# Performance work log

Hardware: AMD Instinct MI355X
Metric: run time of the kernel (lower is better)

Reference implementation:

```python
import jax, jax.numpy as jnp
import numpy as np

T, B, I, H = 512, 256, 256, 512  # seq_len, batch, input_size, hidden_size


def setup_inputs() -> dict:
    key = jax.random.key(0)
    ks = jax.random.split(key, 7)
    sc = 1.0 / np.sqrt(H)  # PyTorch nn.RNN init scale ~ U(-1/sqrt(H), 1/sqrt(H)); use scaled normal
    return {
        "x": jax.random.normal(ks[0], (T, B, I), dtype=jnp.float32),
        "w_ih": jax.random.normal(ks[1], (H, I), dtype=jnp.float32) * sc,
        "w_hh": jax.random.normal(ks[2], (H, H), dtype=jnp.float32) * sc,
        "b_ih": jax.random.normal(ks[3], (H,), dtype=jnp.float32) * sc,
        "b_hh": jax.random.normal(ks[4], (H,), dtype=jnp.float32) * sc,
        "w_fc": jax.random.normal(ks[5], (I, H), dtype=jnp.float32) * sc,
        "b_fc": jax.random.normal(ks[6], (I,), dtype=jnp.float32) * sc,
    }


def reference(x, w_ih, w_hh, b_ih, b_hh, w_fc, b_fc):
    # Single-layer tanh RNN (h0 = 0): h_t = tanh(x_t W_ih^T + b_ih + h_{t-1} W_hh^T + b_hh)
    # Hoist the input projection out of the recurrence (one big GEMM).
    xp = jnp.einsum('tbi,hi->tbh', x, w_ih) + b_ih + b_hh  # [T,B,H]
    h0 = jnp.zeros((x.shape[1], w_hh.shape[0]), dtype=x.dtype)

    def step(h, xt):
        h_new = jnp.tanh(xt + h @ w_hh.T)
        return h_new, h_new

    _, hs = jax.lax.scan(step, h0, xp)  # hs: [T,B,H]
    # Output head: Linear(hidden_size -> input_size)
    return jnp.einsum('tbh,oh->tbo', hs, w_fc) + b_fc  # [T,B,I]
```

## Files before the change

### kernel.cpp

```cpp
#include <hip/hip_runtime.h>
#include <hip/hip_bf16.h>

#define T_ 512
#define B_ 256
#define I_ 256
#define H_ 512

#define NG 16
#define NS 4

#define RING_WPG (H_ * 8)
#define RING_BYTES (2ull * NG * RING_WPG * 8)

typedef _Float16 f16x8 __attribute__((ext_vector_type(8)));
typedef float f32x4 __attribute__((ext_vector_type(4)));

__device__ __forceinline__ float tanh_fast(float v) {
  float e = __expf(2.0f * v);
  return 1.0f - 2.0f / (e + 1.0f);
}

__device__ __forceinline__ f16x8 cvt8(const float4 a, const float4 b) {
  f16x8 f;
  f[0] = (_Float16)a.x; f[1] = (_Float16)a.y; f[2] = (_Float16)a.z; f[3] = (_Float16)a.w;
  f[4] = (_Float16)b.x; f[5] = (_Float16)b.y; f[6] = (_Float16)b.z; f[7] = (_Float16)b.w;
  return f;
}

__device__ __forceinline__ unsigned long long pack2h(_Float16 a, _Float16 b, unsigned tag) {
  unsigned ua = __builtin_bit_cast(unsigned short, a);
  unsigned ub = __builtin_bit_cast(unsigned short, b);
  return (unsigned long long)(ua | (ub << 16)) | ((unsigned long long)tag << 32);
}

__global__ __launch_bounds__(256, 1) void rnn_recurrence(
    const float* __restrict__ x,
    const float* __restrict__ w_ih,
    const float* __restrict__ w_hh,
    const float* __restrict__ b_ih,
    const float* __restrict__ b_hh,
    unsigned long long* __restrict__ ring,
    unsigned long long* __restrict__ ringf,
    _Float16* __restrict__ hs)
{
  const int tid  = threadIdx.x;
  const int lane = tid & 63;
  const int w    = tid >> 6;
  const int bid  = blockIdx.x;
  const int g    = bid & 15;
  const int s    = bid >> 4;
  const int r0   = g * 16;
  const int c0   = s * 128;
  const int lrow = lane & 15;
  const int quad = lane >> 4;
  const int kq   = quad * 8;

  __shared__ _Float16 hbuf[16][512 + 8];
  __shared__ _Float16 xbuf[16][256 + 8];
  __shared__ int g_ok;

  f16x8 whh0[16], whh1[16];
  f16x8 wih0[8], wih1[8];
  const int n0c = c0 + (2 * w + 0) * 16 + lrow;
  const int n1c = c0 + (2 * w + 1) * 16 + lrow;
  const float bias0 = b_ih[n0c] + b_hh[n0c];
  const float bias1 = b_ih[n1c] + b_hh[n1c];
  #pragma unroll
  for (int kt = 0; kt < 16; ++kt) {
    const int pk = (s * 4 + kt) & 15;
    const int k  = pk * 32 + kq;
    whh0[kt] = cvt8(*(const float4*)(w_hh + (size_t)n0c * H_ + k),
                    *(const float4*)(w_hh + (size_t)n0c * H_ + k + 4));
    whh1[kt] = cvt8(*(const float4*)(w_hh + (size_t)n1c * H_ + k),
                    *(const float4*)(w_hh + (size_t)n1c * H_ + k + 4));
  }
  #pragma unroll
  for (int kt = 0; kt < 8; ++kt) {
    const int k = kt * 32 + kq;
    wih0[kt] = cvt8(*(const float4*)(w_ih + (size_t)n0c * I_ + k),
                    *(const float4*)(w_ih + (size_t)n0c * I_ + k + 4));
    wih1[kt] = cvt8(*(const float4*)(w_ih + (size_t)n1c * I_ + k),
                    *(const float4*)(w_ih + (size_t)n1c * I_ + k + 4));
  }

  int roff[12];
  int obyte[12];
  #pragma unroll
  for (int j = 0; j < 12; ++j) {
    const int wdx = tid + j * 256;
    const int rs  = wdx >> 10;
    const int sl  = rs + (rs >= s ? 1 : 0);
    const int c   = (wdx >> 3) & 127;
    const int p   = wdx & 7;
    roff[j]  = (sl * 128 + c) * 8 + p;
    obyte[j] = roff[j] * 8;
  }

  if (tid == 0) g_ok = 1;
  {
    const int row = tid >> 4, ch = tid & 15;
    f16x8 z = {0, 0, 0, 0, 0, 0, 0, 0};
    *(f16x8*)(&hbuf[row][c0 + ch * 8]) = z;
  }
  __syncthreads();

  bool fastmode = true;
  const int xrow = tid >> 5;
  const int xcol = (tid & 31) * 8;

  for (int t = 0; t < T_; ++t) {
    const unsigned ut = (unsigned)t;
    const size_t slot_c = (size_t)((t & 1) ? NG : 0) + g;
    const size_t slot_p = (size_t)(((t + 1) & 1) ? NG : 0) + g;

    const float* src = x + ((size_t)t * B_ + r0) * I_;
    const float4 xv0 = *(const float4*)(src + (size_t)xrow * I_ + xcol);
    const float4 xv1 = *(const float4*)(src + (size_t)xrow * I_ + xcol + 4);
    const float4 xv2 = *(const float4*)(src + (size_t)(xrow + 8) * I_ + xcol);
    const float4 xv3 = *(const float4*)(src + (size_t)(xrow + 8) * I_ + xcol + 4);

    if (t > 0) {
      const int row = tid >> 4, ch = tid & 15;
      *(uint4*)(hs + ((size_t)(t - 1) * B_ + r0 + row) * H_ + c0 + ch * 8) =
          *(const uint4*)(&hbuf[row][c0 + ch * 8]);
    }

    f32x4 a0a = {0.f,0.f,0.f,0.f}, a0b = {0.f,0.f,0.f,0.f};
    f32x4 a1a = {0.f,0.f,0.f,0.f}, a1b = {0.f,0.f,0.f,0.f};
    #pragma unroll
    for (int kt = 0; kt < 4; ++kt) {
      const int pk = (s * 4 + kt) & 15;
      const f16x8 a = *(const f16x8*)(&hbuf[lrow][pk * 32 + kq]);
      a0b = __builtin_amdgcn_mfma_f32_16x16x32_f16(a, whh0[kt], a0b, 0, 0, 0);
      a1b = __builtin_amdgcn_mfma_f32_16x16x32_f16(a, whh1[kt], a1b, 0, 0, 0);
    }

    *(f16x8*)(&xbuf[xrow][xcol])     = cvt8(xv0, xv1);
    *(f16x8*)(&xbuf[xrow + 8][xcol]) = cvt8(xv2, xv3);

    unsigned long long v[12];
    unsigned miss = 0xfffu;
    if (fastmode) {
      const unsigned long long* fb = ringf + slot_c * RING_WPG;
      const int limit = (t <= 1) ? 256 : 0x7fffffff;
      int rounds = 0;
      do {
        asm volatile(
            "global_load_dwordx2 %0, %13, %12 sc0\n\t"
            "global_load_dwordx2 %1, %14, %12 sc0\n\t"
            "global_load_dwordx2 %2, %15, %12 sc0\n\t"
            "global_load_dwordx2 %3, %16, %12 sc0\n\t"
            "global_load_dwordx2 %4, %17, %12 sc0\n\t"
            "global_load_dwordx2 %5, %18, %12 sc0\n\t"
            "global_load_dwordx2 %6, %19, %12 sc0\n\t"
            "global_load_dwordx2 %7, %20, %12 sc0\n\t"
            "global_load_dwordx2 %8, %21, %12 sc0\n\t"
            "global_load_dwordx2 %9, %22, %12 sc0\n\t"
            "global_load_dwordx2 %10, %23, %12 sc0\n\t"
            "global_load_dwordx2 %11, %24, %12 sc0\n\t"
            "s_waitcnt vmcnt(0)"
            : "=&v"(v[0]), "=&v"(v[1]), "=&v"(v[2]), "=&v"(v[3]),
              "=&v"(v[4]), "=&v"(v[5]), "=&v"(v[6]), "=&v"(v[7]),
              "=&v"(v[8]), "=&v"(v[9]), "=&v"(v[10]), "=&v"(v[11])
            : "s"(fb), "v"(obyte[0]), "v"(obyte[1]), "v"(obyte[2]),
              "v"(obyte[3]), "v"(obyte[4]), "v"(obyte[5]), "v"(obyte[6]),
              "v"(obyte[7]), "v"(obyte[8]), "v"(obyte[9]), "v"(obyte[10]),
              "v"(obyte[11])
            : "memory");
        miss = 0u;
        #pragma unroll
        for (int j = 0; j < 12; ++j)
          if ((unsigned)(v[j] >> 32) != ut) miss |= 1u << j;
      } while (miss && ++rounds < limit);
      if (miss) g_ok = 0;
    }
    if (miss) {
      const unsigned long long* rg = ring + slot_c * RING_WPG;
      while (miss) {
        #pragma unroll
        for (int j = 0; j < 12; ++j) {
          if (miss & (1u << j)) {
            const unsigned long long wv = __hip_atomic_load(
                &rg[roff[j]], __ATOMIC_RELAXED, __HIP_MEMORY_SCOPE_AGENT);
            if ((unsigned)(wv >> 32) == ut) { v[j] = wv; miss &= ~(1u << j); }
          }
        }
      }
    }
    #pragma unroll
    for (int j = 0; j < 12; ++j) {
      const int col = roff[j] >> 3;
      const int pr  = (roff[j] & 7) * 2;
      const unsigned lo = (unsigned)v[j];
      hbuf[pr + 0][col] =
          __builtin_bit_cast(_Float16, (unsigned short)(lo & 0xffff));
      hbuf[pr + 1][col] =
          __builtin_bit_cast(_Float16, (unsigned short)(lo >> 16));
    }
    __syncthreads();
    if (t == 1) fastmode = (g_ok != 0);

    #pragma unroll
    for (int kt = 4; kt < 16; ++kt) {
      const int pk = (s * 4 + kt) & 15;
      const f16x8 a = *(const f16x8*)(&hbuf[lrow][pk * 32 + kq]);
      if (kt < 10) {
        a0a = __builtin_amdgcn_mfma_f32_16x16x32_f16(a, whh0[kt], a0a, 0, 0, 0);
        a1a = __builtin_amdgcn_mfma_f32_16x16x32_f16(a, whh1[kt], a1a, 0, 0, 0);
      } else {
        a0b = __builtin_amdgcn_mfma_f32_16x16x32_f16(a, whh0[kt], a0b, 0, 0, 0);
        a1b = __builtin_amdgcn_mfma_f32_16x16x32_f16(a, whh1[kt], a1b, 0, 0, 0);
      }
    }
    #pragma unroll
    for (int kt = 0; kt < 8; ++kt) {
      const f16x8 a = *(const f16x8*)(&xbuf[lrow][kt * 32 + kq]);
      if (kt < 4) {
        a0a = __builtin_amdgcn_mfma_f32_16x16x32_f16(a, wih0[kt], a0a, 0, 0, 0);
        a1a = __builtin_amdgcn_mfma_f32_16x16x32_f16(a, wih1[kt], a1a, 0, 0, 0);
      } else {
        a0b = __builtin_amdgcn_mfma_f32_16x16x32_f16(a, wih0[kt], a0b, 0, 0, 0);
        a1b = __builtin_amdgcn_mfma_f32_16x16x32_f16(a, wih1[kt], a1b, 0, 0, 0);
      }
    }
    const f32x4 acc0 = a0a + a0b;
    const f32x4 acc1 = a1a + a1b;

    _Float16 e0[4], e1[4];
    #pragma unroll
    for (int r = 0; r < 4; ++r) {
      e0[r] = (_Float16)tanh_fast(acc0[r] + bias0);
      e1[r] = (_Float16)tanh_fast(acc1[r] + bias1);
    }
    const unsigned tag = (unsigned)(t + 1);
    if (fastmode) {
      unsigned long long* fn = ringf + slot_p * RING_WPG;
      fn[n0c * 8 + quad * 2 + 0] = pack2h(e0[0], e0[1], tag);
      fn[n0c * 8 + quad * 2 + 1] = pack2h(e0[2], e0[3], tag);
      fn[n1c * 8 + quad * 2 + 0] = pack2h(e1[0], e1[1], tag);
      fn[n1c * 8 + quad * 2 + 1] = pack2h(e1[2], e1[3], tag);
    }
    if (t == 0 || !fastmode) {
      unsigned long long* rn = ring + slot_p * RING_WPG;
      __hip_atomic_store(&rn[n0c * 8 + quad * 2 + 0], pack2h(e0[0], e0[1], tag),
                         __ATOMIC_RELAXED, __HIP_MEMORY_SCOPE_AGENT);
      __hip_atomic_store(&rn[n0c * 8 + quad * 2 + 1], pack2h(e0[2], e0[3], tag),
                         __ATOMIC_RELAXED, __HIP_MEMORY_SCOPE_AGENT);
      __hip_atomic_store(&rn[n1c * 8 + quad * 2 + 0], pack2h(e1[0], e1[1], tag),
                         __ATOMIC_RELAXED, __HIP_MEMORY_SCOPE_AGENT);
      __hip_atomic_store(&rn[n1c * 8 + quad * 2 + 1], pack2h(e1[2], e1[3], tag),
                         __ATOMIC_RELAXED, __HIP_MEMORY_SCOPE_AGENT);
    }
    #pragma unroll
    for (int r = 0; r < 4; ++r) {
      hbuf[quad * 4 + r][n0c] = e0[r];
      hbuf[quad * 4 + r][n1c] = e1[r];
    }
    __syncthreads();
  }

  {
    const int row = tid >> 4, ch = tid & 15;
    *(uint4*)(hs + ((size_t)(T_ - 1) * B_ + r0 + row) * H_ + c0 + ch * 8) =
        *(const uint4*)(&hbuf[row][c0 + ch * 8]);
  }
}

__global__ __launch_bounds__(256) void fc_head(
    const _Float16* __restrict__ hs,
    const float* __restrict__ w_fc,
    const float* __restrict__ b_fc,
    float* __restrict__ out)
{
  const int tid  = threadIdx.x;
  const int lane = tid & 63;
  const int w    = tid >> 6;
  const int wm   = w & 1;
  const int wn   = w >> 1;
  const int m0   = blockIdx.y * 64;
  const int n0   = blockIdx.x * 64;
  const int lrow = lane & 15;
  const int quad = lane >> 4;
  const int kq   = quad * 8;

  __shared__ _Float16 As[64][32 + 8];
  __shared__ _Float16 Bs[64][32 + 8];

  f32x4 acc00 = {0.f,0.f,0.f,0.f}, acc01 = {0.f,0.f,0.f,0.f};
  f32x4 acc10 = {0.f,0.f,0.f,0.f}, acc11 = {0.f,0.f,0.f,0.f};

  const int srow = tid >> 2;
  const int skc  = (tid & 3) * 8;

  for (int k0 = 0; k0 < H_; k0 += 32) {
    *(uint4*)(&As[srow][skc]) =
        *(const uint4*)(hs + (size_t)(m0 + srow) * H_ + k0 + skc);
    *(f16x8*)(&Bs[srow][skc]) =
        cvt8(*(const float4*)(w_fc + (size_t)(n0 + srow) * H_ + k0 + skc),
             *(const float4*)(w_fc + (size_t)(n0 + srow) * H_ + k0 + skc + 4));
    __syncthreads();

    const f16x8 a0 = *(const f16x8*)(&As[wm * 32 + lrow][kq]);
    const f16x8 a1 = *(const f16x8*)(&As[wm * 32 + 16 + lrow][kq]);
    const f16x8 b0 = *(const f16x8*)(&Bs[wn * 32 + lrow][kq]);
    const f16x8 b1 = *(const f16x8*)(&Bs[wn * 32 + 16 + lrow][kq]);
    acc00 = __builtin_amdgcn_mfma_f32_16x16x32_f16(a0, b0, acc00, 0, 0, 0);
    acc01 = __builtin_amdgcn_mfma_f32_16x16x32_f16(a0, b1, acc01, 0, 0, 0);
    acc10 = __builtin_amdgcn_mfma_f32_16x16x32_f16(a1, b0, acc10, 0, 0, 0);
    acc11 = __builtin_amdgcn_mfma_f32_16x16x32_f16(a1, b1, acc11, 0, 0, 0);
    __syncthreads();
  }

  #pragma unroll
  for (int ni = 0; ni < 2; ++ni) {
    const int col = n0 + wn * 32 + ni * 16 + lrow;
    const float bf = b_fc[col];
    #pragma unroll
    for (int mi = 0; mi < 2; ++mi) {
      const f32x4 a = (mi == 0) ? (ni == 0 ? acc00 : acc01)
                                : (ni == 0 ? acc10 : acc11);
      #pragma unroll
      for (int r = 0; r < 4; ++r) {
        const int rowm = m0 + wm * 32 + mi * 16 + quad * 4 + r;
        out[(size_t)rowm * I_ + col] = a[r] + bf;
      }
    }
  }
}

extern "C" void kernel_launch(void* const* d_in, const int* in_sizes, int n_in,
                              void* d_out, int out_size, void* d_ws, size_t ws_size,
                              hipStream_t stream) {
  const float* x    = (const float*)d_in[0];
  const float* w_ih = (const float*)d_in[1];
  const float* w_hh = (const float*)d_in[2];
  const float* b_ih = (const float*)d_in[3];
  const float* b_hh = (const float*)d_in[4];
  const float* w_fc = (const float*)d_in[5];
  const float* b_fc = (const float*)d_in[6];
  float* out = (float*)d_out;

  unsigned long long* ring  = (unsigned long long*)d_ws;
  unsigned long long* ringf = (unsigned long long*)((char*)d_ws + RING_BYTES);
  _Float16* hs = (_Float16*)((char*)d_ws + 2 * RING_BYTES);

  hipMemsetAsync(d_ws, 0, 2 * RING_BYTES, stream);

  rnn_recurrence<<<64, 256, 0, stream>>>(x, w_ih, w_hh, b_ih, b_hh, ring, ringf, hs);
  fc_head<<<dim3(4, 2048), 256, 0, stream>>>(hs, w_fc, b_fc, out);
}
```

Baseline: 1.706 ms.

## Hoist input projection into a separate GEMM and prefetch xp in recurrence

Moves the x·W_ih^T input projection (with both biases) out of the serial recurrence into a parallel fp16 GEMM kernel that writes xp into the output buffer as scratch. The recurrence then loads precomputed xp values into the accumulator init, prefetching the next step's values, and drops the per-step W_ih MFMAs, x loads and xbuf staging. The fast/slow ring mode handling is also changed: the shared flag becomes a per-thread retry budget, both rings are always written, and __syncthreads is replaced by a raw barrier with an lgkm wait. The cost is an extra launch and an fp16 xp round-trip through HBM, and xp is rounded to fp16 before being added to the hidden-state product.

```diff
diff --git a/kernel.cpp b/kernel.cpp
--- a/kernel.cpp
+++ b/kernel.cpp
@@ -33,12 +33,79 @@
   return (unsigned long long)(ua | (ub << 16)) | ((unsigned long long)tag << 32);
 }
 
-__global__ __launch_bounds__(256, 1) void rnn_recurrence(
+__device__ __forceinline__ void barrier_lgkm() {
+  asm volatile("s_waitcnt lgkmcnt(0)" ::: "memory");
+  __builtin_amdgcn_s_barrier();
+  __builtin_amdgcn_sched_barrier(0);
+}
+
+__global__ __launch_bounds__(256) void xp_gemm(
     const float* __restrict__ x,
     const float* __restrict__ w_ih,
-    const float* __restrict__ w_hh,
     const float* __restrict__ b_ih,
     const float* __restrict__ b_hh,
+    _Float16* __restrict__ xp)
+{
+  const int tid  = threadIdx.x;
+  const int lane = tid & 63;
+  const int w    = tid >> 6;
+  const int wm   = w & 1;
+  const int wn   = w >> 1;
+  const int m0   = blockIdx.y * 64;
+  const int n0   = blockIdx.x * 64;
+  const int lrow = lane & 15;
+  const int quad = lane >> 4;
+  const int kq   = quad * 8;
+
+  __shared__ _Float16 As[64][32 + 8];
+  __shared__ _Float16 Bs[64][32 + 8];
+
+  f32x4 acc00 = {0.f,0.f,0.f,0.f}, acc01 = {0.f,0.f,0.f,0.f};
+  f32x4 acc10 = {0.f,0.f,0.f,0.f}, acc11 = {0.f,0.f,0.f,0.f};
+
+  const int srow = tid >> 2;
+  const int skc  = (tid & 3) * 8;
+
+  for (int k0 = 0; k0 < I_; k0 += 32) {
+    *(f16x8*)(&As[srow][skc]) =
+        cvt8(*(const float4*)(x + (size_t)(m0 + srow) * I_ + k0 + skc),
+             *(const float4*)(x + (size_t)(m0 + srow) * I_ + k0 + skc + 4));
+    *(f16x8*)(&Bs[srow][skc]) =
+        cvt8(*(const float4*)(w_ih + (size_t)(n0 + srow) * I_ + k0 + skc),
+             *(const float4*)(w_ih + (size_t)(n0 + srow) * I_ + k0 + skc + 4));
+    __syncthreads();
+
+    const f16x8 a0 = *(const f16x8*)(&As[wm * 32 + lrow][kq]);
+    const f16x8 a1 = *(const f16x8*)(&As[wm * 32 + 16 + lrow][kq]);
+    const f16x8 b0 = *(const f16x8*)(&Bs[wn * 32 + lrow][kq]);
+    const f16x8 b1 = *(const f16x8*)(&Bs[wn * 32 + 16 + lrow][kq]);
+    acc00 = __builtin_amdgcn_mfma_f32_16x16x32_f16(a0, b0, acc00, 0, 0, 0);
+    acc01 = __builtin_amdgcn_mfma_f32_16x16x32_f16(a0, b1, acc01, 0, 0, 0);
+    acc10 = __builtin_amdgcn_mfma_f32_16x16x32_f16(a1, b0, acc10, 0, 0, 0);
+    acc11 = __builtin_amdgcn_mfma_f32_16x16x32_f16(a1, b1, acc11, 0, 0, 0);
+    __syncthreads();
+  }
+
+  #pragma unroll
+  for (int ni = 0; ni < 2; ++ni) {
+    const int col = n0 + wn * 32 + ni * 16 + lrow;
+    const float bf = b_ih[col] + b_hh[col];
+    #pragma unroll
+    for (int mi = 0; mi < 2; ++mi) {
+      const f32x4 a = (mi == 0) ? (ni == 0 ? acc00 : acc01)
+                                : (ni == 0 ? acc10 : acc11);
+      #pragma unroll
+      for (int r = 0; r < 4; ++r) {
+        const int rowm = m0 + wm * 32 + mi * 16 + quad * 4 + r;
+        xp[(size_t)rowm * H_ + col] = (_Float16)(a[r] + bf);
+      }
+    }
+  }
+}
+
+__global__ __launch_bounds__(256, 1) void rnn_recurrence(
+    const _Float16* __restrict__ xp,
+    const float* __restrict__ w_hh,
     unsigned long long* __restrict__ ring,
     unsigned long long* __restrict__ ringf,
     _Float16* __restrict__ hs)
@@ -56,15 +123,10 @@
   const int kq   = quad * 8;
 
   __shared__ _Float16 hbuf[16][512 + 8];
-  __shared__ _Float16 xbuf[16][256 + 8];
-  __shared__ int g_ok;
 
   f16x8 whh0[16], whh1[16];
-  f16x8 wih0[8], wih1[8];
   const int n0c = c0 + (2 * w + 0) * 16 + lrow;
   const int n1c = c0 + (2 * w + 1) * 16 + lrow;
-  const float bias0 = b_ih[n0c] + b_hh[n0c];
-  const float bias1 = b_ih[n1c] + b_hh[n1c];
   #pragma unroll
   for (int kt = 0; kt < 16; ++kt) {
     const int pk = (s * 4 + kt) & 15;
@@ -74,16 +136,7 @@
     whh1[kt] = cvt8(*(const float4*)(w_hh + (size_t)n1c * H_ + k),
                     *(const float4*)(w_hh + (size_t)n1c * H_ + k + 4));
   }
-  #pragma unroll
-  for (int kt = 0; kt < 8; ++kt) {
-    const int k = kt * 32 + kq;
-    wih0[kt] = cvt8(*(const float4*)(w_ih + (size_t)n0c * I_ + k),
-                    *(const float4*)(w_ih + (size_t)n0c * I_ + k + 4));
-    wih1[kt] = cvt8(*(const float4*)(w_ih + (size_t)n1c * I_ + k),
-                    *(const float4*)(w_ih + (size_t)n1c * I_ + k + 4));
-  }
-
-  int roff[12];
+
   int obyte[12];
   #pragma unroll
   for (int j = 0; j < 12; ++j) {
@@ -92,11 +145,9 @@
     const int sl  = rs + (rs >= s ? 1 : 0);
     const int c   = (wdx >> 3) & 127;
     const int p   = wdx & 7;
-    roff[j]  = (sl * 128 + c) * 8 + p;
-    obyte[j] = roff[j] * 8;
-  }
-
-  if (tid == 0) g_ok = 1;
+    obyte[j] = (((sl * 128 + c) * 8) + p) * 8;
+  }
+
   {
     const int row = tid >> 4, ch = tid & 15;
     f16x8 z = {0, 0, 0, 0, 0, 0, 0, 0};
@@ -104,29 +155,30 @@
   }
   __syncthreads();
 
-  bool fastmode = true;
-  const int xrow = tid >> 5;
-  const int xcol = (tid & 31) * 8;
+  unsigned short xs0[4], xs1[4];
+  {
+    const unsigned short* xq = (const unsigned short*)xp + (size_t)r0 * H_;
+    #pragma unroll
+    for (int r = 0; r < 4; ++r) {
+      xs0[r] = xq[(size_t)(quad * 4 + r) * H_ + n0c];
+      xs1[r] = xq[(size_t)(quad * 4 + r) * H_ + n1c];
+    }
+  }
+
+  int fast_budget = 512;
 
   for (int t = 0; t < T_; ++t) {
     const unsigned ut = (unsigned)t;
     const size_t slot_c = (size_t)((t & 1) ? NG : 0) + g;
     const size_t slot_p = (size_t)(((t + 1) & 1) ? NG : 0) + g;
 
-    const float* src = x + ((size_t)t * B_ + r0) * I_;
-    const float4 xv0 = *(const float4*)(src + (size_t)xrow * I_ + xcol);
-    const float4 xv1 = *(const float4*)(src + (size_t)xrow * I_ + xcol + 4);
-    const float4 xv2 = *(const float4*)(src + (size_t)(xrow + 8) * I_ + xcol);
-    const float4 xv3 = *(const float4*)(src + (size_t)(xrow + 8) * I_ + xcol + 4);
-
-    if (t > 0) {
-      const int row = tid >> 4, ch = tid & 15;
-      *(uint4*)(hs + ((size_t)(t - 1) * B_ + r0 + row) * H_ + c0 + ch * 8) =
-          *(const uint4*)(&hbuf[row][c0 + ch * 8]);
-    }
-
-    f32x4 a0a = {0.f,0.f,0.f,0.f}, a0b = {0.f,0.f,0.f,0.f};
-    f32x4 a1a = {0.f,0.f,0.f,0.f}, a1b = {0.f,0.f,0.f,0.f};
+    f32x4 a0a, a1a;
+    #pragma unroll
+    for (int r = 0; r < 4; ++r) {
+      a0a[r] = (float)__builtin_bit_cast(_Float16, xs0[r]);
+      a1a[r] = (float)__builtin_bit_cast(_Float16, xs1[r]);
+    }
+    f32x4 a0b = {0.f,0.f,0.f,0.f}, a1b = {0.f,0.f,0.f,0.f};
     #pragma unroll
     for (int kt = 0; kt < 4; ++kt) {
       const int pk = (s * 4 + kt) & 15;
@@ -135,14 +187,10 @@
       a1b = __builtin_amdgcn_mfma_f32_16x16x32_f16(a, whh1[kt], a1b, 0, 0, 0);
     }
 
-    *(f16x8*)(&xbuf[xrow][xcol])     = cvt8(xv0, xv1);
-    *(f16x8*)(&xbuf[xrow + 8][xcol]) = cvt8(xv2, xv3);
-
     unsigned long long v[12];
     unsigned miss = 0xfffu;
-    if (fastmode) {
+    if (fast_budget > 0) {
       const unsigned long long* fb = ringf + slot_c * RING_WPG;
-      const int limit = (t <= 1) ? 256 : 0x7fffffff;
       int rounds = 0;
       do {
         asm volatile(
@@ -171,8 +219,8 @@
         #pragma unroll
         for (int j = 0; j < 12; ++j)
           if ((unsigned)(v[j] >> 32) != ut) miss |= 1u << j;
-      } while (miss && ++rounds < limit);
-      if (miss) g_ok = 0;
+      } while (miss && ++rounds < fast_budget);
+      if (miss) fast_budget = 0;
     }
     if (miss) {
       const unsigned long long* rg = ring + slot_c * RING_WPG;
@@ -181,24 +229,42 @@
         for (int j = 0; j < 12; ++j) {
           if (miss & (1u << j)) {
             const unsigned long long wv = __hip_atomic_load(
-                &rg[roff[j]], __ATOMIC_RELAXED, __HIP_MEMORY_SCOPE_AGENT);
+                &rg[obyte[j] >> 3], __ATOMIC_RELAXED, __HIP_MEMORY_SCOPE_AGENT);
             if ((unsigned)(wv >> 32) == ut) { v[j] = wv; miss &= ~(1u << j); }
           }
         }
       }
     }
+
     #pragma unroll
     for (int j = 0; j < 12; ++j) {
-      const int col = roff[j] >> 3;
-      const int pr  = (roff[j] & 7) * 2;
+      const int col = obyte[j] >> 6;
+      const int pr  = ((obyte[j] >> 3) & 7) * 2;
       const unsigned lo = (unsigned)v[j];
       hbuf[pr + 0][col] =
           __builtin_bit_cast(_Float16, (unsigned short)(lo & 0xffff));
       hbuf[pr + 1][col] =
           __builtin_bit_cast(_Float16, (unsigned short)(lo >> 16));
     }
-    __syncthreads();
-    if (t == 1) fastmode = (g_ok != 0);
+
+    if (t > 0) {
+      const int row = tid >> 4, ch = tid & 15;
+      *(uint4*)(hs + ((size_t)(t - 1) * B_ + r0 + row) * H_ + c0 + ch * 8) =
+          *(const uint4*)(&hbuf[row][c0 + ch * 8]);
+    }
+
+    {
+      const int tn = (t + 1 < T_) ? (t + 1) : t;
+      const unsigned short* xq =
+          (const unsigned short*)xp + ((size_t)tn * B_ + r0) * H_;
+      #pragma unroll
+      for (int r = 0; r < 4; ++r) {
+        xs0[r] = xq[(size_t)(quad * 4 + r) * H_ + n0c];
+        xs1[r] = xq[(size_t)(quad * 4 + r) * H_ + n1c];
+      }
+    }
+
+    barrier_lgkm();
 
     #pragma unroll
     for (int kt = 4; kt < 16; ++kt) {
@@ -212,35 +278,24 @@
         a1b = __builtin_amdgcn_mfma_f32_16x16x32_f16(a, whh1[kt], a1b, 0, 0, 0);
       }
     }
-    #pragma unroll
-    for (int kt = 0; kt < 8; ++kt) {
-      const f16x8 a = *(const f16x8*)(&xbuf[lrow][kt * 32 + kq]);
-      if (kt < 4) {
-        a0a = __builtin_amdgcn_mfma_f32_16x16x32_f16(a, wih0[kt], a0a, 0, 0, 0);
-        a1a = __builtin_amdgcn_mfma_f32_16x16x32_f16(a, wih1[kt], a1a, 0, 0, 0);
-      } else {
-        a0b = __builtin_amdgcn_mfma_f32_16x16x32_f16(a, wih0[kt], a0b, 0, 0, 0);
-        a1b = __builtin_amdgcn_mfma_f32_16x16x32_f16(a, wih1[kt], a1b, 0, 0, 0);
-      }
-    }
     const f32x4 acc0 = a0a + a0b;
     const f32x4 acc1 = a1a + a1b;
 
     _Float16 e0[4], e1[4];
     #pragma unroll
     for (int r = 0; r < 4; ++r) {
-      e0[r] = (_Float16)tanh_fast(acc0[r] + bias0);
-      e1[r] = (_Float16)tanh_fast(acc1[r] + bias1);
+      e0[r] = (_Float16)tanh_fast(acc0[r]);
+      e1[r] = (_Float16)tanh_fast(acc1[r]);
     }
     const unsigned tag = (unsigned)(t + 1);
-    if (fastmode) {
+    {
       unsigned long long* fn = ringf + slot_p * RING_WPG;
       fn[n0c * 8 + quad * 2 + 0] = pack2h(e0[0], e0[1], tag);
       fn[n0c * 8 + quad * 2 + 1] = pack2h(e0[2], e0[3], tag);
       fn[n1c * 8 + quad * 2 + 0] = pack2h(e1[0], e1[1], tag);
       fn[n1c * 8 + quad * 2 + 1] = pack2h(e1[2], e1[3], tag);
     }
-    if (t == 0 || !fastmode) {
+    {
       unsigned long long* rn = ring + slot_p * RING_WPG;
       __hip_atomic_store(&rn[n0c * 8 + quad * 2 + 0], pack2h(e0[0], e0[1], tag),
                          __ATOMIC_RELAXED, __HIP_MEMORY_SCOPE_AGENT);
@@ -256,7 +311,7 @@
       hbuf[quad * 4 + r][n0c] = e0[r];
       hbuf[quad * 4 + r][n1c] = e1[r];
     }
-    __syncthreads();
+    barrier_lgkm();
   }
 
   {
@@ -343,9 +398,11 @@
   unsigned long long* ring  = (unsigned long long*)d_ws;
   unsigned long long* ringf = (unsigned long long*)((char*)d_ws + RING_BYTES);
   _Float16* hs = (_Float16*)((char*)d_ws + 2 * RING_BYTES);
+  _Float16* xp = (_Float16*)d_out;
 
   hipMemsetAsync(d_ws, 0, 2 * RING_BYTES, stream);
 
-  rnn_recurrence<<<64, 256, 0, stream>>>(x, w_ih, w_hh, b_ih, b_hh, ring, ringf, hs);
+  xp_gemm<<<dim3(H_ / 64, 2048), 256, 0, stream>>>(x, w_ih, b_ih, b_hh, xp);
+  rnn_recurrence<<<64, 256, 0, stream>>>(xp, w_hh, ring, ringf, hs);
   fc_head<<<dim3(4, 2048), 256, 0, stream>>>(hs, w_fc, b_fc, out);
 }
```

Measured after the change: 2.912 ms. +70.8%, slower.
